# Optimization experiments

Measured on AMD Instinct MI355X. Metric: run time of the kernel, lower is better.

The kernel has to match this reference:

```python
import jax, jax.numpy as jnp
import numpy as np

N_NODES = 50000
N_EDGES = 600000
D = 128
HIDDEN = 128
OUT = 1


def setup_inputs() -> dict:
    key = jax.random.key(0)
    ks = jax.random.split(key, 6)
    z = jax.random.normal(ks[0], (N_NODES, D), dtype=jnp.float32)
    e = jax.random.randint(ks[1], (2, N_EDGES), 0, N_NODES, dtype=jnp.int64)
    # Linear weights in [in, out] layout; scaled like torch default init
    W1 = jax.random.normal(ks[2], (2 * D, HIDDEN), dtype=jnp.float32) / np.sqrt(2 * D)
    b1 = jax.random.normal(ks[3], (HIDDEN,), dtype=jnp.float32) / np.sqrt(2 * D)
    W2 = jax.random.normal(ks[4], (HIDDEN, OUT), dtype=jnp.float32) / np.sqrt(HIDDEN)
    b2 = jax.random.normal(ks[5], (OUT,), dtype=jnp.float32) / np.sqrt(HIDDEN)
    return {"z": z, "e": e, "W1": W1, "b1": b1, "W2": W2, "b2": b2}


def reference(z, e, W1, b1, W2, b2):
    x_i = z[e[0]]                      # [E, D] gather source nodes
    x_j = z[e[1]]                      # [E, D] gather target nodes
    x = jnp.concatenate([x_i, x_j], axis=1)  # [E, 2D]
    h = jax.nn.relu(x @ W1 + b1)       # [E, HIDDEN]
    out = h @ W2 + b2                  # [E, OUT]
    return jax.nn.sigmoid(out).squeeze()  # [E]
```

## Files before the change

### kernel.cpp

```cpp
#include <hip/hip_runtime.h>


#define DD 128

typedef __attribute__((ext_vector_type(8))) short short8;
typedef __attribute__((ext_vector_type(4))) float floatx4;

static __device__ __forceinline__ unsigned short f2bf(float f) {
  unsigned int u = __builtin_bit_cast(unsigned int, f);
  u += 0x7fffu + ((u >> 16) & 1u);
  return (unsigned short)(u >> 16);
}
static __device__ __forceinline__ float bflo(unsigned int u) {
  return __builtin_bit_cast(float, u << 16);
}
static __device__ __forceinline__ float bfhi(unsigned int u) {
  return __builtin_bit_cast(float, u & 0xffff0000u);
}

__global__ __launch_bounds__(256) void wt_build(
    const float* __restrict__ W1, unsigned short* __restrict__ Wt) {
  const int g = blockIdx.x * 256 + threadIdx.x;
  const int c = g >> 5;
  const int kq = (g & 31) * 4;
  const float* src = (c < 128) ? (W1 + c) : (W1 + 128 * 128 + (c - 128));
  ushort4 o;
  o.x = f2bf(src[(size_t)(kq + 0) * 128]);
  o.y = f2bf(src[(size_t)(kq + 1) * 128]);
  o.z = f2bf(src[(size_t)(kq + 2) * 128]);
  o.w = f2bf(src[(size_t)(kq + 3) * 128]);
  *(ushort4*)&Wt[c * 128 + kq] = o;
}

__global__ __launch_bounds__(256) void node_mfma(
    const float* __restrict__ z, const unsigned short* __restrict__ Wt,
    const float* __restrict__ b1, unsigned short* __restrict__ gi,
    unsigned short* __restrict__ gj, int n_nodes) {
  __shared__ unsigned short zb[64 * 136];
  const int tid = threadIdx.x;
  const int nb = blockIdx.x * 64;

#pragma unroll
  for (int i = 0; i < 8; ++i) {
    int q = tid + i * 256;
    int nl = q >> 5;
    int node = nb + nl; if (node >= n_nodes) node = n_nodes - 1;
    float4 v = ((const float4*)z)[(size_t)node * 32 + (q & 31)];
    ushort4 o;
    o.x = f2bf(v.x); o.y = f2bf(v.y); o.z = f2bf(v.z); o.w = f2bf(v.w);
    *(ushort4*)&zb[nl * 136 + (q & 31) * 4] = o;
  }

  const int w = tid >> 6, lane = tid & 63;
  const int l15 = lane & 15, quad = lane >> 4;

  short8 a[4][4];
#pragma unroll
  for (int tt = 0; tt < 4; ++tt) {
    const unsigned short* wrow =
        Wt + (size_t)((w * 4 + tt) * 16 + l15) * 128 + quad * 8;
#pragma unroll
    for (int s = 0; s < 4; ++s) a[tt][s] = *(const short8*)(wrow + s * 32);
  }

  floatx4 acc[4][4];
#pragma unroll
  for (int tt = 0; tt < 4; ++tt) {
    floatx4 bias = {0.f, 0.f, 0.f, 0.f};
    if (w < 2) {
      float4 b4 = *(const float4*)&b1[(w * 4 + tt) * 16 + quad * 4];
      bias[0] = b4.x; bias[1] = b4.y; bias[2] = b4.z; bias[3] = b4.w;
    }
#pragma unroll
    for (int nt = 0; nt < 4; ++nt) acc[tt][nt] = bias;
  }

  __syncthreads();

#pragma unroll
  for (int nt = 0; nt < 4; ++nt) {
    short8 bz[4];
#pragma unroll
    for (int s = 0; s < 4; ++s)
      bz[s] = *(const short8*)&zb[(nt * 16 + l15) * 136 + s * 32 + quad * 8];
#pragma unroll
    for (int tt = 0; tt < 4; ++tt)
#pragma unroll
      for (int s = 0; s < 4; ++s)
        acc[tt][nt] =
            __builtin_amdgcn_mfma_f32_16x16x32_bf16(a[tt][s], bz[s], acc[tt][nt], 0, 0, 0);
  }

  unsigned short* base = (w < 2) ? gi : gj;
  const int cbase = w * 64 - ((w < 2) ? 0 : 128);
#pragma unroll
  for (int nt = 0; nt < 4; ++nt) {
    const int node = nb + nt * 16 + l15;
    if (node < n_nodes) {
#pragma unroll
      for (int tt = 0; tt < 4; ++tt) {
        const int c = cbase + tt * 16 + quad * 4;
        ushort4 o;
        o.x = f2bf(acc[tt][nt][0]); o.y = f2bf(acc[tt][nt][1]);
        o.z = f2bf(acc[tt][nt][2]); o.w = f2bf(acc[tt][nt][3]);
        *(ushort4*)&base[(size_t)node * 128 + c] = o;
      }
    }
  }
}

static __device__ __forceinline__ float dot8(uint4 a, uint4 b, float4 w0, float4 w1) {
  float s;
  s = fmaxf(bflo(a.x) + bflo(b.x), 0.f) * w0.x;
  s = fmaf(fmaxf(bfhi(a.x) + bfhi(b.x), 0.f), w0.y, s);
  s = fmaf(fmaxf(bflo(a.y) + bflo(b.y), 0.f), w0.z, s);
  s = fmaf(fmaxf(bfhi(a.y) + bfhi(b.y), 0.f), w0.w, s);
  s = fmaf(fmaxf(bflo(a.z) + bflo(b.z), 0.f), w1.x, s);
  s = fmaf(fmaxf(bfhi(a.z) + bfhi(b.z), 0.f), w1.y, s);
  s = fmaf(fmaxf(bflo(a.w) + bflo(b.w), 0.f), w1.z, s);
  s = fmaf(fmaxf(bfhi(a.w) + bfhi(b.w), 0.f), w1.w, s);
  return s;
}

__global__ __launch_bounds__(256) void edge_mlp(
    const int* __restrict__ e, const unsigned short* __restrict__ gi,
    const unsigned short* __restrict__ gj, const float* __restrict__ W2,
    const float* __restrict__ b2, float* __restrict__ out, int E) {
  const int p = threadIdx.x & 7;
  const float4* wv = (const float4*)W2;
  const float4 w0 = wv[p * 2],      w1 = wv[p * 2 + 1];
  const float4 w2 = wv[16 + p * 2], w3 = wv[16 + p * 2 + 1];
  const float bias2 = b2[0];

  const int stride = gridDim.x * 32;
  for (int edge = blockIdx.x * 32 + (threadIdx.x >> 3); edge < E; edge += stride) {
    const int i = e[edge];
    const int j = e[E + edge];
    const uint4* pi = (const uint4*)(gi + (size_t)i * 128);
    const uint4* pj = (const uint4*)(gj + (size_t)j * 128);
    uint4 a0 = pi[p], a1 = pi[8 + p];
    uint4 c0 = pj[p], c1 = pj[8 + p];
    float acc = dot8(a0, c0, w0, w1) + dot8(a1, c1, w2, w3);
    acc += __shfl_xor(acc, 1);
    acc += __shfl_xor(acc, 2);
    acc += __shfl_xor(acc, 4);
    if (p == 0) {
      float x = acc + bias2;
      out[edge] = 1.f / (1.f + __expf(-x));
    }
  }
}

__global__ __launch_bounds__(256) void edge_direct(
    const int* __restrict__ e, const float* __restrict__ z,
    const float* __restrict__ W1, const float* __restrict__ b1,
    const float* __restrict__ W2, const float* __restrict__ b2,
    float* __restrict__ out, int E) {
  const int lane = threadIdx.x & 63;
  const int edge = (int)((blockIdx.x * 256u + threadIdx.x) >> 6);
  if (edge >= E) return;
  const int i = e[edge], j = e[E + edge];
  const float* zi = z + (size_t)i * 128;
  const float* zj = z + (size_t)j * 128;
  const int c0 = lane * 2;
  float h0 = b1[c0], h1 = b1[c0 + 1];
  for (int k = 0; k < 128; ++k) {
    float a = zi[k], b = zj[k];
    float2 wt = *(const float2*)&W1[(size_t)k * 128 + c0];
    float2 wb = *(const float2*)&W1[(size_t)(128 + k) * 128 + c0];
    h0 = fmaf(a, wt.x, h0); h1 = fmaf(a, wt.y, h1);
    h0 = fmaf(b, wb.x, h0); h1 = fmaf(b, wb.y, h1);
  }
  float s = fmaxf(h0, 0.f) * W2[c0] + fmaxf(h1, 0.f) * W2[c0 + 1];
#pragma unroll
  for (int off = 1; off < 64; off <<= 1) s += __shfl_xor(s, off);
  if (lane == 0) out[edge] = 1.f / (1.f + __expf(-(s + b2[0])));
}

extern "C" void kernel_launch(void* const* d_in, const int* in_sizes, int n_in,
                              void* d_out, int out_size, void* d_ws, size_t ws_size,
                              hipStream_t stream) {
  const float* z  = (const float*)d_in[0];
  const int*   e  = (const int*)d_in[1];
  const float* W1 = (const float*)d_in[2];
  const float* b1 = (const float*)d_in[3];
  const float* W2 = (const float*)d_in[4];
  const float* b2 = (const float*)d_in[5];
  float* out = (float*)d_out;
  const int n_nodes = in_sizes[0] / DD;
  const int E = in_sizes[1] / 2;

  const size_t g_bytes = (size_t)n_nodes * DD * sizeof(unsigned short);
  const size_t wt_bytes = 256 * 128 * sizeof(unsigned short);
  if (ws_size >= 2 * g_bytes + wt_bytes) {
    unsigned short* gi = (unsigned short*)d_ws;
    unsigned short* gj = (unsigned short*)((char*)d_ws + g_bytes);
    unsigned short* Wt = (unsigned short*)((char*)d_ws + 2 * g_bytes);
    wt_build<<<32, 256, 0, stream>>>(W1, Wt);
    node_mfma<<<(n_nodes + 63) / 64, 256, 0, stream>>>(z, Wt, b1, gi, gj, n_nodes);
    edge_mlp<<<2048, 256, 0, stream>>>(e, gi, gj, W2, b2, out, E);
  } else {
    edge_direct<<<(E + 3) / 4, 256, 0, stream>>>(e, z, W1, b1, W2, b2, out, E);
  }
}
```

Measured before the change: 135.6 us.

## Bucket edges by node-index ranges so each XCD gathers from a cache-local slice

Adds an edge_bucket pass that sorts edges into 8x32 buckets keyed by source and target node range. It uses a shared histogram, global atomic offsets and an overflow list. The edge MLP kernel then assigns each XCD (blockIdx & 7) one source-range row of buckets, walking target ranges in order, so the gi and gj rows it gathers stay resident in that XCD's L2. This costs an extra pass over the edge list, scattered output writes, the record buffers and a 16-bit packing limit on node indices. Correctness relies on blockIdx-to-XCD round-robin only for locality, not for results.

```diff
diff --git a/kernel.cpp b/kernel.cpp
--- a/kernel.cpp
+++ b/kernel.cpp
@@ -2,6 +2,10 @@
 
 
 #define DD 128
+#define NBI 8
+#define NBJ 32
+#define NBK (NBI * NBJ)
+#define OVCAP 16384
 
 typedef __attribute__((ext_vector_type(8))) short short8;
 typedef __attribute__((ext_vector_type(4))) float floatx4;
@@ -19,7 +23,10 @@
 }
 
 __global__ __launch_bounds__(256) void wt_build(
-    const float* __restrict__ W1, unsigned short* __restrict__ Wt) {
+    const float* __restrict__ W1, unsigned short* __restrict__ Wt,
+    unsigned int* __restrict__ counters) {
+  if (counters && blockIdx.x == 0 && threadIdx.x <= NBK)
+    counters[threadIdx.x] = 0u;
   const int g = blockIdx.x * 256 + threadIdx.x;
   const int c = g >> 5;
   const int kq = (g & 31) * 4;
@@ -105,6 +112,45 @@
         o.z = f2bf(acc[tt][nt][2]); o.w = f2bf(acc[tt][nt][3]);
         *(ushort4*)&base[(size_t)node * 128 + c] = o;
       }
+    }
+  }
+}
+
+__global__ __launch_bounds__(256) void edge_bucket(
+    const int* __restrict__ e, int E, int ci, int cj, int cap,
+    unsigned int* __restrict__ counters,
+    uint2* __restrict__ recs, uint2* __restrict__ ovrecs) {
+  __shared__ unsigned int hist[NBK];
+  __shared__ unsigned int wbase[NBK];
+  const int tid = threadIdx.x;
+  const int nchunk = (E + gridDim.x - 1) / gridDim.x;
+  const int e0 = blockIdx.x * nchunk;
+  const int e1 = (e0 + nchunk < E) ? (e0 + nchunk) : E;
+  hist[tid] = 0u;
+  __syncthreads();
+  for (int t = e0 + tid; t < e1; t += 256) {
+    const int i = e[t], j = e[E + t];
+    const int key = (i / ci) * NBJ + (j / cj);
+    atomicAdd(&hist[key], 1u);
+  }
+  __syncthreads();
+  const unsigned int h = hist[tid];
+  wbase[tid] = h ? atomicAdd(&counters[tid], h) : 0u;
+  __syncthreads();
+  hist[tid] = 0u;
+  __syncthreads();
+  for (int t = e0 + tid; t < e1; t += 256) {
+    const int i = e[t], j = e[E + t];
+    const int key = (i / ci) * NBJ + (j / cj);
+    const unsigned int off = wbase[key] + atomicAdd(&hist[key], 1u);
+    uint2 r;
+    r.x = (unsigned int)i | ((unsigned int)j << 16);
+    r.y = (unsigned int)t;
+    if (off < (unsigned int)cap) {
+      recs[(size_t)key * cap + off] = r;
+    } else {
+      const unsigned int op = atomicAdd(&counters[NBK], 1u);
+      if (op < OVCAP) ovrecs[op] = r;
     }
   }
 }
@@ -122,6 +168,59 @@
   return s;
 }
 
+__global__ __launch_bounds__(256) void edge_mlp_b(
+    const unsigned short* __restrict__ gi, const unsigned short* __restrict__ gj,
+    const float* __restrict__ W2, const float* __restrict__ b2,
+    float* __restrict__ out,
+    const unsigned int* __restrict__ counters,
+    const uint2* __restrict__ recs, const uint2* __restrict__ ovrecs, int cap) {
+  const int p = threadIdx.x & 7;
+  const float4* wv = (const float4*)W2;
+  const float4 w0 = wv[p * 2],      w1 = wv[p * 2 + 1];
+  const float4 w2 = wv[16 + p * 2], w3 = wv[16 + p * 2 + 1];
+  const float bias2 = b2[0];
+
+  const int xcd = blockIdx.x & 7;
+  const int bslot = blockIdx.x >> 3;
+  const int g = bslot * 32 + (threadIdx.x >> 3);
+
+  for (int jb = 0; jb < NBJ; ++jb) {
+    const int key = xcd * NBJ + jb;
+    int cnt = (int)counters[key]; if (cnt > cap) cnt = cap;
+    const uint2* br = recs + (size_t)key * cap;
+    for (int t = g; t < cnt; t += 8192) {
+      const uint2 r = br[t];
+      const int i = (int)(r.x & 0xffffu);
+      const int j = (int)(r.x >> 16);
+      const uint4* pi = (const uint4*)(gi + (size_t)i * 128);
+      const uint4* pj = (const uint4*)(gj + (size_t)j * 128);
+      uint4 a0 = pi[p], a1 = pi[8 + p];
+      uint4 c0 = pj[p], c1 = pj[8 + p];
+      float acc = dot8(a0, c0, w0, w1) + dot8(a1, c1, w2, w3);
+      acc += __shfl_xor(acc, 1);
+      acc += __shfl_xor(acc, 2);
+      acc += __shfl_xor(acc, 4);
+      if (p == 0) out[r.y] = 1.f / (1.f + __expf(-(acc + bias2)));
+    }
+  }
+
+  int ov = (int)counters[NBK]; if (ov > OVCAP) ov = OVCAP;
+  for (int t = blockIdx.x * 32 + (threadIdx.x >> 3); t < ov; t += gridDim.x * 32) {
+    const uint2 r = ovrecs[t];
+    const int i = (int)(r.x & 0xffffu);
+    const int j = (int)(r.x >> 16);
+    const uint4* pi = (const uint4*)(gi + (size_t)i * 128);
+    const uint4* pj = (const uint4*)(gj + (size_t)j * 128);
+    uint4 a0 = pi[p], a1 = pi[8 + p];
+    uint4 c0 = pj[p], c1 = pj[8 + p];
+    float acc = dot8(a0, c0, w0, w1) + dot8(a1, c1, w2, w3);
+    acc += __shfl_xor(acc, 1);
+    acc += __shfl_xor(acc, 2);
+    acc += __shfl_xor(acc, 4);
+    if (p == 0) out[r.y] = 1.f / (1.f + __expf(-(acc + bias2)));
+  }
+}
+
 __global__ __launch_bounds__(256) void edge_mlp(
     const int* __restrict__ e, const unsigned short* __restrict__ gi,
     const unsigned short* __restrict__ gj, const float* __restrict__ W2,
@@ -131,7 +230,6 @@
   const float4 w0 = wv[p * 2],      w1 = wv[p * 2 + 1];
   const float4 w2 = wv[16 + p * 2], w3 = wv[16 + p * 2 + 1];
   const float bias2 = b2[0];
-
   const int stride = gridDim.x * 32;
   for (int edge = blockIdx.x * 32 + (threadIdx.x >> 3); edge < E; edge += stride) {
     const int i = e[edge];
@@ -144,10 +242,7 @@
     acc += __shfl_xor(acc, 1);
     acc += __shfl_xor(acc, 2);
     acc += __shfl_xor(acc, 4);
-    if (p == 0) {
-      float x = acc + bias2;
-      out[edge] = 1.f / (1.f + __expf(-x));
-    }
+    if (p == 0) out[edge] = 1.f / (1.f + __expf(-(acc + bias2)));
   }
 }
 
@@ -192,11 +287,33 @@
 
   const size_t g_bytes = (size_t)n_nodes * DD * sizeof(unsigned short);
   const size_t wt_bytes = 256 * 128 * sizeof(unsigned short);
-  if (ws_size >= 2 * g_bytes + wt_bytes) {
+  const int cap = E / NBK * 2 + 2048;
+  const size_t cnt_bytes = 2048;
+  const size_t rec_bytes = (size_t)NBK * cap * sizeof(uint2);
+  const size_t ov_bytes = (size_t)OVCAP * sizeof(uint2);
+  const size_t need_bucketed =
+      2 * g_bytes + wt_bytes + cnt_bytes + rec_bytes + ov_bytes;
+
+  if (ws_size >= need_bucketed && n_nodes <= 65535 && n_nodes > 0) {
     unsigned short* gi = (unsigned short*)d_ws;
     unsigned short* gj = (unsigned short*)((char*)d_ws + g_bytes);
     unsigned short* Wt = (unsigned short*)((char*)d_ws + 2 * g_bytes);
-    wt_build<<<32, 256, 0, stream>>>(W1, Wt);
+    unsigned int* counters =
+        (unsigned int*)((char*)d_ws + 2 * g_bytes + wt_bytes);
+    uint2* recs = (uint2*)((char*)d_ws + 2 * g_bytes + wt_bytes + cnt_bytes);
+    uint2* ovrecs = (uint2*)((char*)recs + rec_bytes);
+    const int ci = (n_nodes + NBI - 1) / NBI;
+    const int cj = (n_nodes + NBJ - 1) / NBJ;
+    wt_build<<<32, 256, 0, stream>>>(W1, Wt, counters);
+    edge_bucket<<<256, 256, 0, stream>>>(e, E, ci, cj, cap, counters, recs, ovrecs);
+    node_mfma<<<(n_nodes + 63) / 64, 256, 0, stream>>>(z, Wt, b1, gi, gj, n_nodes);
+    edge_mlp_b<<<2048, 256, 0, stream>>>(gi, gj, W2, b2, out, counters, recs,
+                                         ovrecs, cap);
+  } else if (ws_size >= 2 * g_bytes + wt_bytes) {
+    unsigned short* gi = (unsigned short*)d_ws;
+    unsigned short* gj = (unsigned short*)((char*)d_ws + g_bytes);
+    unsigned short* Wt = (unsigned short*)((char*)d_ws + 2 * g_bytes);
+    wt_build<<<32, 256, 0, stream>>>(W1, Wt, nullptr);
     node_mfma<<<(n_nodes + 63) / 64, 256, 0, stream>>>(z, Wt, b1, gi, gj, n_nodes);
     edge_mlp<<<2048, 256, 0, stream>>>(e, gi, gj, W2, b2, out, E);
   } else {
```

Result: slower. 158.3 us (+16.7%).
